# Kernel tuning notes

Measured on AMD Instinct MI355X. Metric: run time of the kernel, lower is better.

Reference implementation:

```python
import jax, jax.numpy as jnp
import numpy as np

SEQ, D_IN, D_OUT = 4096, 1024, 1024

def setup_inputs() -> dict:
    key = jax.random.key(0)
    kx, kq, kk, kv = jax.random.split(key, 4)
    s = 1.0 / np.sqrt(D_IN)
    return {
        "x": jax.random.normal(kx, (SEQ, D_IN), dtype=jnp.float32),
        "Wq": jax.random.uniform(kq, (D_IN, D_OUT), dtype=jnp.float32, minval=-s, maxval=s),
        "Wk": jax.random.uniform(kk, (D_IN, D_OUT), dtype=jnp.float32, minval=-s, maxval=s),
        "Wv": jax.random.uniform(kv, (D_IN, D_OUT), dtype=jnp.float32, minval=-s, maxval=s),
    }

def reference(x, Wq, Wk, Wv):
    # Single-head self-attention on a 2-D input [S, d_in].
    q = x @ Wq  # [S, d_out]
    k = x @ Wk
    v = x @ Wv
    scale = 1.0 / jnp.sqrt(jnp.asarray(k.shape[-1], dtype=q.dtype))
    attn = jax.nn.softmax(jnp.einsum('sd,td->st', q, k) * scale, axis=-1)  # [S, S]
    return attn @ v  # [S, d_out]
```

## Files before the change

### kernel.cpp

```cpp
#include <hip/hip_runtime.h>
#include <stdint.h>

typedef __bf16 bf16;
typedef __bf16 bf16x8 __attribute__((ext_vector_type(8)));
typedef __bf16 bf16x4 __attribute__((ext_vector_type(4)));
typedef float  f32x4  __attribute__((ext_vector_type(4)));

#define DEVINL __device__ __forceinline__

DEVINL void gload_lds16(const void* g, void* l) {
  __builtin_amdgcn_global_load_lds(
      (const __attribute__((address_space(1))) uint32_t*)g,
      (__attribute__((address_space(3))) uint32_t*)l, 16, 0, 0);
}

DEVINL void swizzle_xy(int& bx, int& by) {
  const int gx = gridDim.x, gy = gridDim.y;
  const int nwg = gx * gy;
  int lin = blockIdx.y * gx + blockIdx.x;
  if ((nwg & 7) == 0) lin = (lin & 7) * (nwg >> 3) + (lin >> 3);
  bx = lin % gx; by = lin / gx;
}

template<int BM, int BN, int BK>
DEVINL void gemm_core(const bf16* __restrict__ A, const bf16* __restrict__ Bt,
                      int K, int row0, int col0,
                      bf16* As, bf16* Bs, f32x4 (&acc)[BM/32][BN/32])
{
  constexpr int FM = BM / 32, FN = BN / 32;
  constexpr int RB  = BK * 2;
  constexpr int IA  = BM * RB / 4096;
  constexpr int IB  = BN * RB / 4096;
  constexpr int RPI = 4096 / RB;
  const int t = threadIdx.x;
  const int wave = t >> 6, lane = t & 63;

  const int sL   = t * 16;
  const int srow = sL / RB;
  const int scb  = (sL % RB) ^ ((srow & 7) << 4);
  const bf16* gA = A  + (size_t)(row0 + srow) * K + (scb >> 1);
  const bf16* gB = Bt + (size_t)(col0 + srow) * K + (scb >> 1);

  const int wr = (wave >> 1) * (BM / 2);
  const int wc = (wave & 1)  * (BN / 2);
  const int fr = lane & 15, kg16 = (lane >> 4) * 16;
  const int arow = wr + fr, brow = wc + fr;
  const int aswz = (arow & 7) << 4;
  const int bswz = (brow & 7) << 4;

  #pragma unroll
  for (int i = 0; i < FM; i++)
    #pragma unroll
    for (int j = 0; j < FN; j++)
      acc[i][j] = f32x4{0.f, 0.f, 0.f, 0.f};

  for (int kt = 0; kt < K; kt += BK) {
    #pragma unroll
    for (int i = 0; i < IA; i++)
      gload_lds16(gA + (size_t)i * RPI * K, (char*)As + i * 4096 + sL);
    #pragma unroll
    for (int i = 0; i < IB; i++)
      gload_lds16(gB + (size_t)i * RPI * K, (char*)Bs + i * 4096 + sL);
    gA += BK; gB += BK;
    __syncthreads();
    #pragma unroll
    for (int kk = 0; kk < BK / 32; kk++) {
      bf16x8 af[FM], bfr[FN];
      #pragma unroll
      for (int m = 0; m < FM; m++)
        af[m] = *(const bf16x8*)((const char*)As + (arow + m * 16) * RB
                                 + ((kk * 64 + kg16) ^ aswz));
      #pragma unroll
      for (int n = 0; n < FN; n++)
        bfr[n] = *(const bf16x8*)((const char*)Bs + (brow + n * 16) * RB
                                  + ((kk * 64 + kg16) ^ bswz));
      #pragma unroll
      for (int m = 0; m < FM; m++)
        #pragma unroll
        for (int n = 0; n < FN; n++)
          acc[m][n] = __builtin_amdgcn_mfma_f32_16x16x32_bf16(af[m], bfr[n], acc[m][n], 0, 0, 0);
    }
    __syncthreads();
  }
}

template<int BM, int BN, int MODE>
__global__ __launch_bounds__(256)
void gemm_bt(const bf16* __restrict__ A, const bf16* __restrict__ Bt,
             void* __restrict__ Cout, int K, int ldc)
{
  __shared__ __align__(16) bf16 As[BM * 64];
  __shared__ __align__(16) bf16 Bs[BN * 64];
  int bx, by; swizzle_xy(bx, by);
  const int row0 = by * BM, col0 = bx * BN;
  f32x4 acc[BM / 32][BN / 32];
  gemm_core<BM, BN, 64>(A, Bt, K, row0, col0, As, Bs, acc);

  const int wave = threadIdx.x >> 6, lane = threadIdx.x & 63;
  const int wr = (wave >> 1) * (BM / 2), wc = (wave & 1) * (BN / 2);
  const int ec = lane & 15, er = (lane >> 4) * 4;
  #pragma unroll
  for (int m = 0; m < BM / 32; m++)
    #pragma unroll
    for (int n = 0; n < BN / 32; n++) {
      const int r = row0 + wr + m * 16 + er;
      const int c = col0 + wc + n * 16 + ec;
      if constexpr (MODE == 0) {
        bf16* C = (bf16*)Cout;
        #pragma unroll
        for (int j = 0; j < 4; j++)
          C[(size_t)(r + j) * ldc + c] = (bf16)acc[m][n][j];
      } else {
        float* C = (float*)Cout;
        #pragma unroll
        for (int j = 0; j < 4; j++)
          C[(size_t)(r + j) * ldc + c] = acc[m][n][j];
      }
    }
}

__global__ __launch_bounds__(256)
void gemm_qkv(const bf16* __restrict__ xb, const bf16* __restrict__ Wt,
              bf16* __restrict__ Qb, bf16* __restrict__ Kb, bf16* __restrict__ Vt)
{
  __shared__ __align__(16) bf16 As[128 * 64];
  __shared__ __align__(16) bf16 Bs[128 * 64];
  const int z = blockIdx.z;
  int bx, by; swizzle_xy(bx, by);
  const int row0 = by * 128, col0 = bx * 128;
  f32x4 acc[4][4];
  gemm_core<128, 128, 64>(xb, Wt + (size_t)z * 1024 * 1024, 1024, row0, col0, As, Bs, acc);

  const int wave = threadIdx.x >> 6, lane = threadIdx.x & 63;
  const int wr = (wave >> 1) * 64, wc = (wave & 1) * 64;
  const int ec = lane & 15, er = (lane >> 4) * 4;
  if (z == 2) {
    #pragma unroll
    for (int m = 0; m < 4; m++)
      #pragma unroll
      for (int n = 0; n < 4; n++) {
        const int r = row0 + wr + m * 16 + er;
        const int c = col0 + wc + n * 16 + ec;
        bf16x4 pk;
        #pragma unroll
        for (int j = 0; j < 4; j++) pk[j] = (bf16)acc[m][n][j];
        *(bf16x4*)(Vt + (size_t)c * 4096 + r) = pk;
      }
  } else {
    bf16* C = z ? Kb : Qb;
    const float sc = z ? 1.0f : 0.03125f;
    #pragma unroll
    for (int m = 0; m < 4; m++)
      #pragma unroll
      for (int n = 0; n < 4; n++) {
        const int r = row0 + wr + m * 16 + er;
        const int c = col0 + wc + n * 16 + ec;
        #pragma unroll
        for (int j = 0; j < 4; j++)
          C[(size_t)(r + j) * 1024 + c] = (bf16)(acc[m][n][j] * sc);
      }
  }
}

__global__ __launch_bounds__(256)
void softmax_inplace(bf16* __restrict__ S)
{
  const int t = threadIdx.x;
  bf16* p = S + (size_t)blockIdx.x * 4096 + t * 16;
  bf16x8 v0 = *(const bf16x8*)p;
  bf16x8 v1 = *(const bf16x8*)(p + 8);
  float f[16];
  #pragma unroll
  for (int j = 0; j < 8; j++) { f[j] = (float)v0[j]; f[8 + j] = (float)v1[j]; }
  float mx = f[0];
  #pragma unroll
  for (int j = 1; j < 16; j++) mx = fmaxf(mx, f[j]);
  #pragma unroll
  for (int off = 32; off > 0; off >>= 1) mx = fmaxf(mx, __shfl_xor(mx, off));
  __shared__ float rmax[4], rsum[4];
  const int wave = t >> 6, lane = t & 63;
  if (lane == 0) rmax[wave] = mx;
  __syncthreads();
  mx = fmaxf(fmaxf(rmax[0], rmax[1]), fmaxf(rmax[2], rmax[3]));
  float s = 0.f;
  #pragma unroll
  for (int j = 0; j < 16; j++) { f[j] = __expf(f[j] - mx); s += f[j]; }
  #pragma unroll
  for (int off = 32; off > 0; off >>= 1) s += __shfl_xor(s, off);
  if (lane == 0) rsum[wave] = s;
  __syncthreads();
  const float inv = 1.f / (rsum[0] + rsum[1] + rsum[2] + rsum[3]);
  #pragma unroll
  for (int j = 0; j < 8; j++) {
    v0[j] = (bf16)(f[j] * inv);
    v1[j] = (bf16)(f[8 + j] * inv);
  }
  *(bf16x8*)p = v0;
  *(bf16x8*)(p + 8) = v1;
}

__global__ __launch_bounds__(256)
void cvt_f32_bf16(const float* __restrict__ in, bf16* __restrict__ o)
{
  const size_t i = ((size_t)blockIdx.x * 256 + threadIdx.x) * 8;
  const float4 a = *(const float4*)(in + i);
  const float4 b = *(const float4*)(in + i + 4);
  bf16x8 v;
  v[0] = (bf16)a.x; v[1] = (bf16)a.y; v[2] = (bf16)a.z; v[3] = (bf16)a.w;
  v[4] = (bf16)b.x; v[5] = (bf16)b.y; v[6] = (bf16)b.z; v[7] = (bf16)b.w;
  *(bf16x8*)(o + i) = v;
}

__global__ __launch_bounds__(256)
void transpose_cvt(const float* __restrict__ Wq, const float* __restrict__ Wk,
                   const float* __restrict__ Wv, bf16* __restrict__ Wt)
{
  const float* W = blockIdx.z == 0 ? Wq : (blockIdx.z == 1 ? Wk : Wv);
  bf16* O = Wt + (size_t)blockIdx.z * 1024 * 1024;
  __shared__ bf16 tile[64][65];
  const int tx = threadIdx.x & 63;
  const int tg = threadIdx.x >> 6;
  const int r0 = blockIdx.y * 64;
  const int c0 = blockIdx.x * 64;
  #pragma unroll
  for (int i = 0; i < 16; i++) {
    const int r = i * 4 + tg;
    tile[tx][r] = (bf16)W[(size_t)(r0 + r) * 1024 + c0 + tx];
  }
  __syncthreads();
  #pragma unroll
  for (int i = 0; i < 16; i++) {
    const int rr = i * 4 + tg;
    O[(size_t)(c0 + rr) * 1024 + r0 + tx] = tile[rr][tx];
  }
}

extern "C" void kernel_launch(void* const* d_in, const int* in_sizes, int n_in,
                              void* d_out, int out_size, void* d_ws, size_t ws_size,
                              hipStream_t stream)
{
  const float* x  = (const float*)d_in[0];
  const float* Wq = (const float*)d_in[1];
  const float* Wk = (const float*)d_in[2];
  const float* Wv = (const float*)d_in[3];
  char* ws = (char*)d_ws;
  const size_t MB = 1024 * 1024;
  bf16* xb = (bf16*)(ws);
  bf16* Wt = (bf16*)(ws +  8 * MB);
  bf16* Qb = (bf16*)(ws + 14 * MB);
  bf16* Kb = (bf16*)(ws + 22 * MB);
  bf16* Vt = (bf16*)(ws + 30 * MB);
  bf16* S  = (bf16*)(ws + 38 * MB);

  cvt_f32_bf16   <<<dim3(2048),      dim3(256), 0, stream>>>(x, xb);
  transpose_cvt  <<<dim3(16, 16, 3), dim3(256), 0, stream>>>(Wq, Wk, Wv, Wt);
  gemm_qkv       <<<dim3(8, 32, 3),  dim3(256), 0, stream>>>(xb, Wt, Qb, Kb, Vt);
  gemm_bt<128, 128, 0><<<dim3(32, 32), dim3(256), 0, stream>>>(Qb, Kb, (void*)S, 1024, 4096);
  softmax_inplace<<<dim3(4096),      dim3(256), 0, stream>>>(S);
  gemm_bt<128, 64, 1><<<dim3(16, 32), dim3(256), 0, stream>>>(S, Vt, (void*)d_out, 4096, 1024);
}
```

Baseline: 241.9 us.

## Double-buffer LDS tiles in GEMM core and adjust BK and swizzle

Restructures the GEMM main loop to double-buffer the LDS tiles, so the global-to-LDS loads for the next K tile are issued before the MFMA work on the current tile. This drops one barrier per iteration and aims to hide global load latency. To keep LDS usage in check, BK drops to 32 for the QKV and QK^T GEMMs, and the swizzle function is generalised to suit the narrower rows. The cost is twice the LDS per block at the same BK, plus more loop iterations wherever BK was halved.

```diff
diff --git a/kernel.cpp b/kernel.cpp
--- a/kernel.cpp
+++ b/kernel.cpp
@@ -22,6 +22,9 @@
   bx = lin % gx; by = lin / gx;
 }
 
+template<int SWM>
+DEVINL int swz(int r) { return ((r ^ (r >> 2)) & SWM) << 4; }
+
 template<int BM, int BN, int BK>
 DEVINL void gemm_core(const bf16* __restrict__ A, const bf16* __restrict__ Bt,
                       int K, int row0, int col0,
@@ -29,24 +32,24 @@
 {
   constexpr int FM = BM / 32, FN = BN / 32;
   constexpr int RB  = BK * 2;
+  constexpr int SWM = (RB / 16) - 1 > 7 ? 7 : (RB / 16) - 1;
   constexpr int IA  = BM * RB / 4096;
   constexpr int IB  = BN * RB / 4096;
   constexpr int RPI = 4096 / RB;
-  const int t = threadIdx.x;
-  const int wave = t >> 6, lane = t & 63;
-
-  const int sL   = t * 16;
+  constexpr int ABY = BM * BK * 2;
+  constexpr int BBY = BN * BK * 2;
+  const int tid = threadIdx.x;
+  const int wave = tid >> 6, lane = tid & 63;
+
+  const int sL   = tid * 16;
   const int srow = sL / RB;
-  const int scb  = (sL % RB) ^ ((srow & 7) << 4);
+  const int scb  = (sL % RB) ^ swz<SWM>(srow);
   const bf16* gA = A  + (size_t)(row0 + srow) * K + (scb >> 1);
   const bf16* gB = Bt + (size_t)(col0 + srow) * K + (scb >> 1);
 
   const int wr = (wave >> 1) * (BM / 2);
   const int wc = (wave & 1)  * (BN / 2);
   const int fr = lane & 15, kg16 = (lane >> 4) * 16;
-  const int arow = wr + fr, brow = wc + fr;
-  const int aswz = (arow & 7) << 4;
-  const int bswz = (brow & 7) << 4;
 
   #pragma unroll
   for (int i = 0; i < FM; i++)
@@ -54,47 +57,60 @@
     for (int j = 0; j < FN; j++)
       acc[i][j] = f32x4{0.f, 0.f, 0.f, 0.f};
 
-  for (int kt = 0; kt < K; kt += BK) {
+  auto stage = [&](int buf, int ti) {
+    const bf16* ga = gA + (size_t)ti * BK;
+    const bf16* gb = gB + (size_t)ti * BK;
     #pragma unroll
     for (int i = 0; i < IA; i++)
-      gload_lds16(gA + (size_t)i * RPI * K, (char*)As + i * 4096 + sL);
+      gload_lds16(ga + (size_t)i * RPI * K, (char*)As + buf * ABY + i * 4096 + sL);
     #pragma unroll
     for (int i = 0; i < IB; i++)
-      gload_lds16(gB + (size_t)i * RPI * K, (char*)Bs + i * 4096 + sL);
-    gA += BK; gB += BK;
-    __syncthreads();
-    #pragma unroll
-    for (int kk = 0; kk < BK / 32; kk++) {
-      bf16x8 af[FM], bfr[FN];
+      gload_lds16(gb + (size_t)i * RPI * K, (char*)Bs + buf * BBY + i * 4096 + sL);
+  };
+
+  const int nt = K / BK;
+  stage(0, 0);
+  __syncthreads();
+  int cur = 0;
+  for (int ti = 0; ti < nt; ++ti) {
+    if (ti + 1 < nt) stage(cur ^ 1, ti + 1);
+    const char* aB = (const char*)As + cur * ABY;
+    const char* bB = (const char*)Bs + cur * BBY;
+    #pragma unroll
+    for (int kk = 0; kk < BK / 32; ++kk) {
+      bf16x8 af[FM], bg[FN];
+      #pragma unroll
+      for (int m = 0; m < FM; m++) {
+        const int r = wr + fr + m * 16;
+        af[m] = *(const bf16x8*)(aB + r * RB + ((kk * 64 + kg16) ^ swz<SWM>(r)));
+      }
+      #pragma unroll
+      for (int n = 0; n < FN; n++) {
+        const int r = wc + fr + n * 16;
+        bg[n] = *(const bf16x8*)(bB + r * RB + ((kk * 64 + kg16) ^ swz<SWM>(r)));
+      }
       #pragma unroll
       for (int m = 0; m < FM; m++)
-        af[m] = *(const bf16x8*)((const char*)As + (arow + m * 16) * RB
-                                 + ((kk * 64 + kg16) ^ aswz));
-      #pragma unroll
-      for (int n = 0; n < FN; n++)
-        bfr[n] = *(const bf16x8*)((const char*)Bs + (brow + n * 16) * RB
-                                  + ((kk * 64 + kg16) ^ bswz));
-      #pragma unroll
-      for (int m = 0; m < FM; m++)
         #pragma unroll
         for (int n = 0; n < FN; n++)
-          acc[m][n] = __builtin_amdgcn_mfma_f32_16x16x32_bf16(af[m], bfr[n], acc[m][n], 0, 0, 0);
+          acc[m][n] = __builtin_amdgcn_mfma_f32_16x16x32_bf16(af[m], bg[n], acc[m][n], 0, 0, 0);
     }
     __syncthreads();
-  }
-}
-
-template<int BM, int BN, int MODE>
+    cur ^= 1;
+  }
+}
+
+template<int BM, int BN, int BK, int MODE>
 __global__ __launch_bounds__(256)
 void gemm_bt(const bf16* __restrict__ A, const bf16* __restrict__ Bt,
              void* __restrict__ Cout, int K, int ldc)
 {
-  __shared__ __align__(16) bf16 As[BM * 64];
-  __shared__ __align__(16) bf16 Bs[BN * 64];
+  __shared__ __align__(16) bf16 As[2 * BM * BK];
+  __shared__ __align__(16) bf16 Bs[2 * BN * BK];
   int bx, by; swizzle_xy(bx, by);
   const int row0 = by * BM, col0 = bx * BN;
   f32x4 acc[BM / 32][BN / 32];
-  gemm_core<BM, BN, 64>(A, Bt, K, row0, col0, As, Bs, acc);
+  gemm_core<BM, BN, BK>(A, Bt, K, row0, col0, As, Bs, acc);
 
   const int wave = threadIdx.x >> 6, lane = threadIdx.x & 63;
   const int wr = (wave >> 1) * (BM / 2), wc = (wave & 1) * (BN / 2);
@@ -123,13 +139,13 @@
 void gemm_qkv(const bf16* __restrict__ xb, const bf16* __restrict__ Wt,
               bf16* __restrict__ Qb, bf16* __restrict__ Kb, bf16* __restrict__ Vt)
 {
-  __shared__ __align__(16) bf16 As[128 * 64];
-  __shared__ __align__(16) bf16 Bs[128 * 64];
+  __shared__ __align__(16) bf16 As[2 * 128 * 32];
+  __shared__ __align__(16) bf16 Bs[2 * 128 * 32];
   const int z = blockIdx.z;
   int bx, by; swizzle_xy(bx, by);
   const int row0 = by * 128, col0 = bx * 128;
   f32x4 acc[4][4];
-  gemm_core<128, 128, 64>(xb, Wt + (size_t)z * 1024 * 1024, 1024, row0, col0, As, Bs, acc);
+  gemm_core<128, 128, 32>(xb, Wt + (size_t)z * 1024 * 1024, 1024, row0, col0, As, Bs, acc);
 
   const int wave = threadIdx.x >> 6, lane = threadIdx.x & 63;
   const int wr = (wave >> 1) * 64, wc = (wave & 1) * 64;
@@ -255,7 +271,7 @@
   cvt_f32_bf16   <<<dim3(2048),      dim3(256), 0, stream>>>(x, xb);
   transpose_cvt  <<<dim3(16, 16, 3), dim3(256), 0, stream>>>(Wq, Wk, Wv, Wt);
   gemm_qkv       <<<dim3(8, 32, 3),  dim3(256), 0, stream>>>(xb, Wt, Qb, Kb, Vt);
-  gemm_bt<128, 128, 0><<<dim3(32, 32), dim3(256), 0, stream>>>(Qb, Kb, (void*)S, 1024, 4096);
+  gemm_bt<128, 128, 32, 0><<<dim3(32, 32), dim3(256), 0, stream>>>(Qb, Kb, (void*)S, 1024, 4096);
   softmax_inplace<<<dim3(4096),      dim3(256), 0, stream>>>(S);
-  gemm_bt<128, 64, 1><<<dim3(16, 32), dim3(256), 0, stream>>>(S, Vt, (void*)d_out, 4096, 1024);
-}
+  gemm_bt<128, 64, 64, 1><<<dim3(16, 32), dim3(256), 0, stream>>>(S, Vt, (void*)d_out, 4096, 1024);
+}
```

New measurement: 221.9 us. 1.09x faster.
